# Kernel optimization log

Measured on AMD Instinct MI355X. Metric: run time of the kernel, lower is better.

## Reference

```python
import jax, jax.numpy as jnp
import numpy as np

B, S, D = 8, 2048, 1024
N = 256          # state_dim
H = 512          # selector_hidden
E = 8            # num_experts


def murmurhash3_finalizer(token_ids):
    # Torch code works in int64 but masks to 32 bits after each multiply and
    # values stay non-negative, so it is exactly uint32 wrapping arithmetic.
    x = token_ids.astype(jnp.uint32)
    x = x ^ (x >> 16)
    x = x * jnp.uint32(2246822507)
    x = x ^ (x >> 13)
    x = x * jnp.uint32(3266489909)
    x = x ^ (x >> 16)
    return x


def setup_inputs() -> dict:
    key = jax.random.key(0)
    ks = jax.random.split(key, 7)
    scale = 0.02
    return {
        "x": jax.random.normal(ks[0], (B, S, D), dtype=jnp.float32),
        "token_ids": jax.random.randint(ks[1], (B, S), 0, 50257, dtype=jnp.int32),
        "Win": jax.random.normal(ks[2], (E, N, D), dtype=jnp.float32) * scale,      # in_proj.weight per expert
        "Wsin": jax.random.normal(ks[3], (E, H, D), dtype=jnp.float32) * scale,     # selector_in.weight
        "Wsout": jax.random.normal(ks[4], (E, 4 * N, H), dtype=jnp.float32) * scale,  # selector_out.weight
        "Wout": jax.random.normal(ks[5], (E, D, N), dtype=jnp.float32) * scale,     # out_proj.weight
        "dparam": jnp.ones((E, N), dtype=jnp.float32),                              # per-expert d
    }


def _forward(x, Win, Wsin, Wsout, Wout, dparam, token_ids):
    b, s, d = x.shape
    e_num, n, _ = Win.shape
    routes = (murmurhash3_finalizer(token_ids) % jnp.uint32(e_num)).astype(jnp.int32)  # (B,S)

    # Per-token expert projections, selected by hash route (masked accumulation
    # over the small fixed expert count; honors per-token routing).
    u = jnp.zeros((b, s, n), x.dtype)
    a = jnp.zeros((b, s, n), x.dtype)
    bg = jnp.zeros((b, s, n), x.dtype)
    c = jnp.zeros((b, s, n), x.dtype)
    dg = jnp.zeros((b, s, n), x.dtype)
    for e in range(e_num):
        m = (routes == e)[..., None]
        u = jnp.where(m, jnp.einsum('bsd,nd->bsn', x, Win[e]), u)
        sh = jax.nn.silu(jnp.einsum('bsd,hd->bsh', x, Wsin[e]))
        sel = jnp.einsum('bsh,oh->bso', sh, Wsout[e])       # (B,S,4N)
        ar, br, cr, dr = jnp.split(sel, 4, axis=-1)
        a = jnp.where(m, jax.nn.sigmoid(ar), a)
        bg = jnp.where(m, jnp.tanh(br), bg)
        c = jnp.where(m, jnp.tanh(cr), c)
        dg = jnp.where(m, jax.nn.sigmoid(dr), dg)

    dvec = dparam[routes]              # (B,S,N) expert d param per token
    skip = dvec * dg * u               # residual term, state-independent

    bidx = jnp.arange(b)

    def step(states, inp):
        # states: (B,E,N) per-expert hidden state per batch row
        route_t, u_t, a_t, b_t, c_t, skip_t = inp
        h_prev = states[bidx, route_t]                 # (B,N)
        h = a_t * h_prev + b_t * u_t
        states = states.at[bidx, route_t].set(h)       # only routed expert updates
        y = c_t * h + skip_t
        return states, y

    xs = (routes.swapaxes(0, 1), u.swapaxes(0, 1), a.swapaxes(0, 1),
          bg.swapaxes(0, 1), c.swapaxes(0, 1), skip.swapaxes(0, 1))
    states0 = jnp.zeros((b, e_num, n), x.dtype)
    _, ys = jax.lax.scan(step, states0, xs)            # ys: (S,B,N)
    y = ys.swapaxes(0, 1)                              # (B,S,N)

    out = jnp.zeros((b, s, d), x.dtype)
    for e in range(e_num):
        m = (routes == e)[..., None]
        out = jnp.where(m, jnp.einsum('bsn,dn->bsd', y, Wout[e]), out)
    return out


def reference(x, token_ids, Win, Wsin, Wsout, Wout, dparam):
    return _forward(x, Win, Wsin, Wsout, Wout, dparam, token_ids)
```

## Files before the change

### kernel.cpp

```cpp
#include <hip/hip_runtime.h>


#define TOKS 16384
#define RPAD 16512
#define DD   1024
#define NN   256
#define HH   512
#define MAXTILES  136
#define MAXCHUNKS 1088
#define CHUNK 16

typedef short short8 __attribute__((ext_vector_type(8)));
typedef float floatx4 __attribute__((ext_vector_type(4)));
typedef _Float16 half_t;

#define AS_GLOBAL __attribute__((address_space(1)))
#define AS_LDS    __attribute__((address_space(3)))

__device__ __forceinline__ void gl_lds16(const void* g, void* l) {
    __builtin_amdgcn_global_load_lds((const AS_GLOBAL void*)g, (AS_LDS void*)l, 16, 0, 0);
}

__device__ __forceinline__ unsigned short f2bf(float f) {
    union { float f; unsigned u; } c; c.f = f;
    unsigned r = c.u + 0x7FFF + ((c.u >> 16) & 1);
    return (unsigned short)(r >> 16);
}
__device__ __forceinline__ int route_of(int token) {
    unsigned x = (unsigned)token;
    x ^= x >> 16; x *= 2246822507u; x ^= x >> 13; x *= 3266489909u; x ^= x >> 16;
    return (int)(x & 7u);
}
__device__ __forceinline__ float sigm(float v) { return 1.0f / (1.0f + __expf(-v)); }
__device__ __forceinline__ float ftanh(float v) {
    float e = __expf(2.0f * v);
    return 1.0f - 2.0f / (e + 1.0f);
}

__global__ void k_route(const int* __restrict__ tok, int* __restrict__ cnt) {
    int b = blockIdx.x, tid = threadIdx.x;
    __shared__ int lc[256 * 8];
    #pragma unroll
    for (int e = 0; e < 8; e++) lc[tid * 8 + e] = 0;
    #pragma unroll
    for (int i = 0; i < 8; i++) {
        int e = route_of(tok[b * 2048 + tid * 8 + i]);
        lc[tid * 8 + e]++;
    }
    __syncthreads();
    if (tid < 8) {
        int s = 0;
        for (int t = 0; t < 256; t++) s += lc[t * 8 + tid];
        cnt[b * 8 + tid] = s;
    }
}

__global__ void k_offsets(const int* __restrict__ cnt, int* __restrict__ grpoff,
                          int* __restrict__ tileE, int* __restrict__ tileS,
                          int* __restrict__ tileR,
                          int* __restrict__ cGrp, int* __restrict__ cStart,
                          int* __restrict__ cLen, int* __restrict__ gBase,
                          int* __restrict__ meta) {
    __shared__ int sc[64], ce[8], eoff[9], etile[9], gb[65], go[64];
    int tid = threadIdx.x;
    if (tid < 64) sc[tid] = cnt[tid];
    __syncthreads();
    if (tid < 8) { int s = 0; for (int b = 0; b < 8; b++) s += sc[b * 8 + tid]; ce[tid] = s; }
    __syncthreads();
    if (tid == 0) {
        eoff[0] = 0; etile[0] = 0;
        for (int e = 0; e < 8; e++) {
            eoff[e + 1] = eoff[e] + ce[e];
            etile[e + 1] = etile[e] + (ce[e] + 127) / 128;
        }
        meta[0] = etile[8];
        gb[0] = 0;
        for (int g = 0; g < 64; g++) gb[g + 1] = gb[g] + (sc[g] + CHUNK - 1) / CHUNK;
        meta[1] = gb[64];
    }
    __syncthreads();
    if (tid < 64) {
        int b = tid >> 3, e = tid & 7;
        int run = eoff[e];
        for (int b2 = 0; b2 < b; b2++) run += sc[b2 * 8 + e];
        go[tid] = run;
        grpoff[tid] = run;
    }
    __syncthreads();
    if (tid < 8) {
        int e = tid, st = eoff[e], c = ce[e], t0 = etile[e];
        for (int i = 0, k = 0; i < c; i += 128, k++) {
            tileE[t0 + k] = e; tileS[t0 + k] = st + i;
            tileR[t0 + k] = (c - i < 128) ? (c - i) : 128;
        }
    }
    if (tid < 64) {
        int g = tid, n = sc[g], base = gb[g], s0 = go[g];
        gBase[g] = base;
        for (int i = 0, c = 0; i < n; i += CHUNK, c++) {
            cGrp[base + c] = g;
            cStart[base + c] = s0 + i;
            cLen[base + c] = (n - i < CHUNK) ? (n - i) : CHUNK;
        }
    }
}

__global__ void k_scatter(const int* __restrict__ tok, const int* __restrict__ grpoff,
                          int* __restrict__ perm) {
    int b = blockIdx.x, tid = threadIdx.x;
    __shared__ int lh[8 * 256];
    int r[8];
    int myc[8] = {0,0,0,0,0,0,0,0};
    #pragma unroll
    for (int i = 0; i < 8; i++) {
        int e = route_of(tok[b * 2048 + tid * 8 + i]);
        r[i] = e; myc[e]++;
    }
    #pragma unroll
    for (int e = 0; e < 8; e++) lh[e * 256 + tid] = myc[e];
    __syncthreads();
    for (int e = 0; e < 8; e++) {
        for (int off = 1; off < 256; off <<= 1) {
            int add = (tid >= off) ? lh[e * 256 + tid - off] : 0;
            __syncthreads();
            lh[e * 256 + tid] += add;
            __syncthreads();
        }
    }
    int basep[8];
    #pragma unroll
    for (int e = 0; e < 8; e++) basep[e] = grpoff[b * 8 + e] + lh[e * 256 + tid] - myc[e];
    #pragma unroll
    for (int i = 0; i < 8; i++) {
        int e = r[i];
        perm[basep[e]++] = b * 2048 + tid * 8 + i;
    }
}

__global__ void k_cvtw(const float* __restrict__ Win, const float* __restrict__ Wsin,
                       const float* __restrict__ Wsout, const float* __restrict__ Wout,
                       unsigned short* __restrict__ W12, unsigned short* __restrict__ Wso,
                       unsigned short* __restrict__ Wo) {
    const int C12 = 8 * 768 * 1024 / 4, CSO = 8 * 1024 * 512 / 4, CWO = 8 * 1024 * 256 / 4;
    int c = blockIdx.x * 256 + threadIdx.x;
    float4 v; unsigned short* dst;
    if (c < C12) {
        int d = c * 4;
        int e = d / (768 * 1024);
        int rem = d - e * (768 * 1024);
        int r = rem >> 10, k = rem & 1023;
        const float* src = (r < 256) ? (Win + (((size_t)e * 256 + r) << 10) + k)
                                     : (Wsin + (((size_t)e * 512 + (r - 256)) << 10) + k);
        v = *(const float4*)src;
        dst = W12 + d;
    } else if (c < C12 + CSO) {
        int d = (c - C12) * 4;
        v = *(const float4*)(Wsout + d);
        dst = Wso + d;
    } else if (c < C12 + CSO + CWO) {
        int d = (c - C12 - CSO) * 4;
        v = *(const float4*)(Wout + d);
        dst = Wo + d;
    } else return;
    ushort4 o;
    o.x = f2bf(v.x); o.y = f2bf(v.y); o.z = f2bf(v.z); o.w = f2bf(v.w);
    *(ushort4*)dst = o;
}

__global__ void k_gather(const float* __restrict__ x, const int* __restrict__ perm,
                         unsigned short* __restrict__ Xs, unsigned short* __restrict__ SHb,
                         unsigned short* __restrict__ Yb) {
    int r = blockIdx.x, t = threadIdx.x;
    if (r < TOKS) {
        int tok = perm[r];
        float4 v = *(const float4*)(x + (size_t)tok * 1024 + t * 4);
        ushort4 o;
        o.x = f2bf(v.x); o.y = f2bf(v.y); o.z = f2bf(v.z); o.w = f2bf(v.w);
        *(ushort4*)(Xs + (size_t)r * 1024 + t * 4) = o;
    } else {
        ushort4 z = {0, 0, 0, 0};
        *(ushort4*)(Xs + (size_t)r * 1024 + t * 4) = z;
        if (t < 128) *(ushort4*)(SHb + (size_t)r * 512 + t * 4) = z;
        if (t < 64)  *(ushort4*)(Yb + (size_t)r * 256 + t * 4) = z;
    }
}

template<int MODE, int KD>
__global__ __launch_bounds__(256, 5)
void k_mfma(const unsigned short* __restrict__ A, const unsigned short* __restrict__ Bw,
            const int* __restrict__ perm, const float* __restrict__ dparam,
            half_t* __restrict__ Ub, unsigned short* __restrict__ SHb,
            half_t* __restrict__ Aa, half_t* __restrict__ Wg,
            half_t* __restrict__ Cc, half_t* __restrict__ Sk,
            float* __restrict__ out,
            const int* __restrict__ tileE, const int* __restrict__ tileS,
            const int* __restrict__ tileR, const int* __restrict__ meta) {
    const int mt = blockIdx.y;
    if (mt >= meta[0]) return;
    const int e = tileE[mt], pos0 = tileS[mt], rows = tileR[mt];
    const int col0 = blockIdx.x * 128;
    const int tid = threadIdx.x;
    const int w = tid >> 6, lane = tid & 63, quad = lane >> 4, l15 = lane & 15;
    const int wm = w & 1, wn = w >> 1;
    constexpr int NOUT = (MODE == 0) ? 768 : 1024;
    constexpr int NK = KD / 32;

    __shared__ unsigned short As[2][128 * 32];
    __shared__ unsigned short Bs[2][128 * 32];

    const int r0 = tid >> 2;
    const int c8s = ((tid & 3) ^ ((tid >> 3) & 3)) * 8;
    const unsigned short* ga = A + (size_t)(pos0 + r0) * KD + c8s;
    const unsigned short* gb = Bw + ((size_t)e * NOUT + col0 + r0) * KD + c8s;

    floatx4 acc[4][4] = {};

    const int sq = (quad ^ ((l15 >> 1) & 3)) * 8;
    int aoff[4], boff[4];
    #pragma unroll
    for (int i = 0; i < 4; i++) aoff[i] = (wm * 64 + i * 16 + l15) * 32 + sq;
    #pragma unroll
    for (int j = 0; j < 4; j++) boff[j] = (wn * 64 + j * 16 + l15) * 32 + sq;

    #define STAGE(buf, k0) do { \
        gl_lds16(ga + (k0),                    As[buf] + w * 512); \
        gl_lds16(ga + (size_t)64 * KD + (k0),  As[buf] + 2048 + w * 512); \
        gl_lds16(gb + (k0),                    Bs[buf] + w * 512); \
        gl_lds16(gb + (size_t)64 * KD + (k0),  Bs[buf] + 2048 + w * 512); \
    } while (0)

    STAGE(0, 0);
    for (int kt = 0; kt < NK; kt++) {
        const int cur = kt & 1;
        if (kt + 1 < NK) {
            STAGE(cur ^ 1, (kt + 1) * 32);
            asm volatile("s_waitcnt vmcnt(4)" ::: "memory");
        } else {
            asm volatile("s_waitcnt vmcnt(0)" ::: "memory");
        }
        __builtin_amdgcn_s_barrier();
        asm volatile("" ::: "memory");
        short8 af[4], bf[4];
        #pragma unroll
        for (int i = 0; i < 4; i++) af[i] = *(const short8*)(As[cur] + aoff[i]);
        #pragma unroll
        for (int j = 0; j < 4; j++) bf[j] = *(const short8*)(Bs[cur] + boff[j]);
        #pragma unroll
        for (int i = 0; i < 4; i++)
            #pragma unroll
            for (int j = 0; j < 4; j++)
                acc[i][j] = __builtin_amdgcn_mfma_f32_16x16x32_bf16(af[i], bf[j], acc[i][j], 0, 0, 0);
        if (kt + 1 < NK) {
            asm volatile("s_waitcnt lgkmcnt(0)" ::: "memory");
            __builtin_amdgcn_s_barrier();
        }
    }
    #undef STAGE
    asm volatile("" ::: "memory");

    #pragma unroll
    for (int i = 0; i < 4; i++) {
        #pragma unroll
        for (int r = 0; r < 4; r++) {
            int m = wm * 64 + i * 16 + quad * 4 + r;
            if (m >= rows) continue;
            size_t row = (size_t)(pos0 + m);
            if (MODE == 0) {
                if (col0 < 256) {
                    #pragma unroll
                    for (int j = 0; j < 4; j++) {
                        int n = col0 + wn * 64 + j * 16 + l15;
                        Ub[row * 256 + n] = (half_t)acc[i][j][r];
                    }
                } else {
                    #pragma unroll
                    for (int j = 0; j < 4; j++) {
                        int n = col0 - 256 + wn * 64 + j * 16 + l15;
                        float v = acc[i][j][r];
                        SHb[row * 512 + n] = f2bf(v * sigm(v));
                    }
                }
            } else if (MODE == 1) {
                int region = col0 >> 8;
                #pragma unroll
                for (int j = 0; j < 4; j++) {
                    int n0 = (col0 & 255) + wn * 64 + j * 16 + l15;
                    size_t idx = row * 256 + (size_t)n0;
                    float v = acc[i][j][r];
                    if (region == 0) {
                        Aa[idx] = (half_t)sigm(v);
                    } else if (region == 1) {
                        Wg[idx] = (half_t)(ftanh(v) * (float)Ub[idx]);
                    } else if (region == 2) {
                        Cc[idx] = (half_t)ftanh(v);
                    } else {
                        Sk[idx] = (half_t)(dparam[e * 256 + n0] * sigm(v) * (float)Ub[idx]);
                    }
                }
            } else {
                int tok = perm[row];
                #pragma unroll
                for (int j = 0; j < 4; j++) {
                    int n = col0 + wn * 64 + j * 16 + l15;
                    out[(size_t)tok * 1024 + n] = acc[i][j][r];
                }
            }
        }
    }
}

__global__ void k_scanA(const half_t* __restrict__ Aa, const half_t* __restrict__ Wg,
                        const int* __restrict__ cStart, const int* __restrict__ cLen,
                        const int* __restrict__ meta,
                        float* __restrict__ SA, float* __restrict__ SQ) {
    int id = blockIdx.x;
    if (id >= meta[1]) return;
    int t = threadIdx.x;
    int s0 = cStart[id], L = cLen[id];
    size_t idx = (size_t)s0 * 256 + t;
    float p = 1.0f, q = 0.0f;
    for (int i = 0; i < L; i++) {
        float a = (float)Aa[idx], ww = (float)Wg[idx];
        q = a * q + ww;
        p *= a;
        idx += 256;
    }
    SA[(size_t)id * 256 + t] = p;
    SQ[(size_t)id * 256 + t] = q;
}

__global__ void k_scanB(const float* __restrict__ SA, const float* __restrict__ SQ,
                        const int* __restrict__ gBase, const int* __restrict__ cnt,
                        float* __restrict__ Hin) {
    int g = blockIdx.x, t = threadIdx.x;
    int base = gBase[g], nch = (cnt[g] + CHUNK - 1) / CHUNK;
    float h = 0.0f;
    for (int c = 0; c < nch; c++) {
        size_t k = (size_t)(base + c) * 256 + t;
        Hin[k] = h;
        h = SA[k] * h + SQ[k];
    }
}

__global__ void k_scanC(const half_t* __restrict__ Aa, const half_t* __restrict__ Wg,
                        const half_t* __restrict__ Cc, const half_t* __restrict__ Sk,
                        const int* __restrict__ cStart, const int* __restrict__ cLen,
                        const int* __restrict__ meta, const float* __restrict__ Hin,
                        unsigned short* __restrict__ Yb) {
    int id = blockIdx.x;
    if (id >= meta[1]) return;
    int t = threadIdx.x;
    int s0 = cStart[id], L = cLen[id];
    float h = Hin[(size_t)id * 256 + t];
    size_t idx = (size_t)s0 * 256 + t;
    for (int i = 0; i < L; i++) {
        float a = (float)Aa[idx], ww = (float)Wg[idx];
        float c = (float)Cc[idx], sk = (float)Sk[idx];
        h = a * h + ww;
        Yb[idx] = f2bf(c * h + sk);
        idx += 256;
    }
}

extern "C" void kernel_launch(void* const* d_in, const int* in_sizes, int n_in,
                              void* d_out, int out_size, void* d_ws, size_t ws_size,
                              hipStream_t stream) {
    const float* xin   = (const float*)d_in[0];
    const int*   tok   = (const int*)d_in[1];
    const float* Win   = (const float*)d_in[2];
    const float* Wsin  = (const float*)d_in[3];
    const float* Wsout = (const float*)d_in[4];
    const float* Wout  = (const float*)d_in[5];
    const float* dpar  = (const float*)d_in[6];
    float* out = (float*)d_out;

    size_t off = 0;
    char* base = (char*)d_ws;
    auto alloc = [&](size_t bytes) -> void* {
        void* p = base + off;
        off += (bytes + 255) & ~(size_t)255;
        return p;
    };
    half_t*         Ub  = (half_t*)alloc((size_t)RPAD * NN * 2);
    unsigned short* SHb = (unsigned short*)alloc((size_t)RPAD * HH * 2);
    unsigned short* Xs  = (unsigned short*)alloc((size_t)RPAD * DD * 2);
    unsigned short* Yb  = (unsigned short*)alloc((size_t)RPAD * NN * 2);
    half_t* Aa = (half_t*)alloc((size_t)TOKS * NN * 2);
    half_t* Wg = (half_t*)alloc((size_t)TOKS * NN * 2);
    half_t* Cc = (half_t*)alloc((size_t)TOKS * NN * 2);
    half_t* Sk = (half_t*)alloc((size_t)TOKS * NN * 2);
    unsigned short* W12 = (unsigned short*)alloc((size_t)8 * 768 * 1024 * 2);
    unsigned short* Wso = (unsigned short*)alloc((size_t)8 * 1024 * 512 * 2);
    unsigned short* Wo  = (unsigned short*)alloc((size_t)8 * 1024 * 256 * 2);
    float* SA  = (float*)alloc((size_t)MAXCHUNKS * 256 * 4);
    float* SQ  = (float*)alloc((size_t)MAXCHUNKS * 256 * 4);
    float* Hin = (float*)alloc((size_t)MAXCHUNKS * 256 * 4);
    int* perm   = (int*)alloc(TOKS * 4);
    int* cnt    = (int*)alloc(64 * 4);
    int* grpoff = (int*)alloc(64 * 4);
    int* tileE  = (int*)alloc(MAXTILES * 4);
    int* tileS  = (int*)alloc(MAXTILES * 4);
    int* tileR  = (int*)alloc(MAXTILES * 4);
    int* cGrp   = (int*)alloc(MAXCHUNKS * 4);
    int* cStart = (int*)alloc(MAXCHUNKS * 4);
    int* cLen   = (int*)alloc(MAXCHUNKS * 4);
    int* gBase  = (int*)alloc(64 * 4);
    int* meta   = (int*)alloc(16 * 4);

    k_route<<<8, 256, 0, stream>>>(tok, cnt);
    k_offsets<<<1, 256, 0, stream>>>(cnt, grpoff, tileE, tileS, tileR,
                                     cGrp, cStart, cLen, gBase, meta);
    k_scatter<<<8, 256, 0, stream>>>(tok, grpoff, perm);
    k_cvtw<<<12288, 256, 0, stream>>>(Win, Wsin, Wsout, Wout, W12, Wso, Wo);
    k_gather<<<RPAD, 256, 0, stream>>>(xin, perm, Xs, SHb, Yb);

    k_mfma<0, 1024><<<dim3(6, MAXTILES), 256, 0, stream>>>(Xs, W12, perm, dpar,
        Ub, SHb, Aa, Wg, Cc, Sk, out, tileE, tileS, tileR, meta);
    k_mfma<1, 512><<<dim3(8, MAXTILES), 256, 0, stream>>>(SHb, Wso, perm, dpar,
        Ub, SHb, Aa, Wg, Cc, Sk, out, tileE, tileS, tileR, meta);

    k_scanA<<<MAXCHUNKS, 256, 0, stream>>>(Aa, Wg, cStart, cLen, meta, SA, SQ);
    k_scanB<<<64, 256, 0, stream>>>(SA, SQ, gBase, cnt, Hin);
    k_scanC<<<MAXCHUNKS, 256, 0, stream>>>(Aa, Wg, Cc, Sk, cStart, cLen, meta, Hin, Yb);

    k_mfma<2, 256><<<dim3(8, MAXTILES), 256, 0, stream>>>(Yb, Wo, perm, dpar,
        Ub, SHb, Aa, Wg, Cc, Sk, out, tileE, tileS, tileR, meta);
}
```

Baseline: 366.1 us.

## Keep A tile resident in LDS and stream weight column blocks per workgroup

The grouped MFMA GEMM now loads the whole K-extent of the activation tile into LDS once. Each workgroup then loops over several 128-column weight blocks through a triple-buffered B pipeline, instead of reloading A for every column block. The first GEMM switches to 64-row tiles, one workgroup per tile covering all 768 outputs. The other two use 512-thread workgroups covering 4 column blocks each. This cuts redundant activation traffic and launch width, at the cost of large LDS footprints, lower occupancy, and fewer workgroups, which may leave CUs underused.

```diff
diff --git a/kernel.cpp b/kernel.cpp
--- a/kernel.cpp
+++ b/kernel.cpp
@@ -7,6 +7,7 @@
 #define NN   256
 #define HH   512
 #define MAXTILES  136
+#define MAXT64    272
 #define MAXCHUNKS 1088
 #define CHUNK 16
 
@@ -58,22 +59,26 @@
 __global__ void k_offsets(const int* __restrict__ cnt, int* __restrict__ grpoff,
                           int* __restrict__ tileE, int* __restrict__ tileS,
                           int* __restrict__ tileR,
+                          int* __restrict__ tE64, int* __restrict__ tS64,
+                          int* __restrict__ tR64,
                           int* __restrict__ cGrp, int* __restrict__ cStart,
                           int* __restrict__ cLen, int* __restrict__ gBase,
                           int* __restrict__ meta) {
-    __shared__ int sc[64], ce[8], eoff[9], etile[9], gb[65], go[64];
+    __shared__ int sc[64], ce[8], eoff[9], etile[9], et64[9], gb[65], go[64];
     int tid = threadIdx.x;
     if (tid < 64) sc[tid] = cnt[tid];
     __syncthreads();
     if (tid < 8) { int s = 0; for (int b = 0; b < 8; b++) s += sc[b * 8 + tid]; ce[tid] = s; }
     __syncthreads();
     if (tid == 0) {
-        eoff[0] = 0; etile[0] = 0;
+        eoff[0] = 0; etile[0] = 0; et64[0] = 0;
         for (int e = 0; e < 8; e++) {
             eoff[e + 1] = eoff[e] + ce[e];
             etile[e + 1] = etile[e] + (ce[e] + 127) / 128;
+            et64[e + 1] = et64[e] + (ce[e] + 63) / 64;
         }
         meta[0] = etile[8];
+        meta[2] = et64[8];
         gb[0] = 0;
         for (int g = 0; g < 64; g++) gb[g + 1] = gb[g] + (sc[g] + CHUNK - 1) / CHUNK;
         meta[1] = gb[64];
@@ -92,6 +97,13 @@
         for (int i = 0, k = 0; i < c; i += 128, k++) {
             tileE[t0 + k] = e; tileS[t0 + k] = st + i;
             tileR[t0 + k] = (c - i < 128) ? (c - i) : 128;
+        }
+    }
+    if (tid >= 8 && tid < 16) {
+        int e = tid - 8, st = eoff[e], c = ce[e], t0 = et64[e];
+        for (int i = 0, k = 0; i < c; i += 64, k++) {
+            tE64[t0 + k] = e; tS64[t0 + k] = st + i;
+            tR64[t0 + k] = (c - i < 64) ? (c - i) : 64;
         }
     }
     if (tid < 64) {
@@ -185,128 +197,153 @@
     }
 }
 
-template<int MODE, int KD>
-__global__ __launch_bounds__(256, 5)
+template<int MODE, int KD, int BM, int THR, int COLS_PB, int MIDX, int MINW>
+__global__ __launch_bounds__(THR, MINW)
 void k_mfma(const unsigned short* __restrict__ A, const unsigned short* __restrict__ Bw,
             const int* __restrict__ perm, const float* __restrict__ dparam,
             half_t* __restrict__ Ub, unsigned short* __restrict__ SHb,
             half_t* __restrict__ Aa, half_t* __restrict__ Wg,
             half_t* __restrict__ Cc, half_t* __restrict__ Sk,
             float* __restrict__ out,
-            const int* __restrict__ tileE, const int* __restrict__ tileS,
-            const int* __restrict__ tileR, const int* __restrict__ meta) {
-    const int mt = blockIdx.y;
-    if (mt >= meta[0]) return;
-    const int e = tileE[mt], pos0 = tileS[mt], rows = tileR[mt];
-    const int col0 = blockIdx.x * 128;
+            const int* __restrict__ tE, const int* __restrict__ tS,
+            const int* __restrict__ tR, const int* __restrict__ meta) {
+    constexpr int NKS  = KD / 32;
+    constexpr int LOGK = (NKS == 32) ? 5 : (NKS == 16) ? 4 : 3;
+    constexpr int ASTR = BM * 32;
+    constexpr int NOUT = (MODE == 0) ? 768 : 1024;
+    constexpr int WM   = BM / 64;
+    constexpr int TOT  = COLS_PB * NKS;
+    constexpr int BL   = 8192 / (THR * 16);
+
+    const int mt = (MODE == 0) ? blockIdx.x : blockIdx.y;
+    if (mt >= meta[MIDX]) return;
+    const int e = tE[mt], pos0 = tS[mt], rows = tR[mt];
+    const int colbase = (MODE == 0) ? 0 : blockIdx.x * (COLS_PB * 128);
     const int tid = threadIdx.x;
     const int w = tid >> 6, lane = tid & 63, quad = lane >> 4, l15 = lane & 15;
-    const int wm = w & 1, wn = w >> 1;
-    constexpr int NOUT = (MODE == 0) ? 768 : 1024;
-    constexpr int NK = KD / 32;
-
-    __shared__ unsigned short As[2][128 * 32];
-    __shared__ unsigned short Bs[2][128 * 32];
+    const int wm = (WM == 2) ? (w & 1) : 0;
+    const int wn = (WM == 2) ? (w >> 1) : w;
+
+    __shared__ unsigned short Ares[NKS * ASTR];
+    __shared__ unsigned short Bs[3][128 * 32];
 
     const int r0 = tid >> 2;
     const int c8s = ((tid & 3) ^ ((tid >> 3) & 3)) * 8;
-    const unsigned short* ga = A + (size_t)(pos0 + r0) * KD + c8s;
-    const unsigned short* gb = Bw + ((size_t)e * NOUT + col0 + r0) * KD + c8s;
-
-    floatx4 acc[4][4] = {};
+    const unsigned short* ga  = A + (size_t)(pos0 + r0) * KD + c8s;
+    const unsigned short* gbb = Bw + ((size_t)e * NOUT + colbase + r0) * KD + c8s;
 
     const int sq = (quad ^ ((l15 >> 1) & 3)) * 8;
-    int aoff[4], boff[4];
+    int aoff[4], boff[2];
     #pragma unroll
     for (int i = 0; i < 4; i++) aoff[i] = (wm * 64 + i * 16 + l15) * 32 + sq;
     #pragma unroll
-    for (int j = 0; j < 4; j++) boff[j] = (wn * 64 + j * 16 + l15) * 32 + sq;
-
-    #define STAGE(buf, k0) do { \
-        gl_lds16(ga + (k0),                    As[buf] + w * 512); \
-        gl_lds16(ga + (size_t)64 * KD + (k0),  As[buf] + 2048 + w * 512); \
-        gl_lds16(gb + (k0),                    Bs[buf] + w * 512); \
-        gl_lds16(gb + (size_t)64 * KD + (k0),  Bs[buf] + 2048 + w * 512); \
+    for (int j = 0; j < 2; j++) boff[j] = (wn * 32 + j * 16 + l15) * 32 + sq;
+
+    #define STAGE_B(buf, s) do { \
+        int cc_ = (s) >> LOGK, ks_ = (s) & (NKS - 1); \
+        const unsigned short* p_ = gbb + (size_t)cc_ * (128 * KD) + ks_ * 32; \
+        gl_lds16(p_, Bs[buf] + w * 512); \
+        if (BL == 2) gl_lds16(p_ + (size_t)64 * KD, Bs[buf] + 2048 + w * 512); \
     } while (0)
 
-    STAGE(0, 0);
-    for (int kt = 0; kt < NK; kt++) {
-        const int cur = kt & 1;
-        if (kt + 1 < NK) {
-            STAGE(cur ^ 1, (kt + 1) * 32);
-            asm volatile("s_waitcnt vmcnt(4)" ::: "memory");
-        } else {
-            asm volatile("s_waitcnt vmcnt(0)" ::: "memory");
+    #pragma unroll
+    for (int s = 0; s < NKS; s++)
+        gl_lds16(ga + s * 32, Ares + s * ASTR + w * 512);
+    STAGE_B(0, 0);
+    STAGE_B(1, 1);
+    asm volatile("s_waitcnt vmcnt(0)" ::: "memory");
+    __builtin_amdgcn_s_barrier();
+
+    floatx4 acc[4][2] = {};
+
+    #pragma unroll 1
+    for (int s = 0; s < TOT; s++) {
+        const int ks = s & (NKS - 1);
+        const int buf = s % 3;
+        if (s > 1) {
+            if (s < TOT - 1) {
+                if (BL == 2) asm volatile("s_waitcnt vmcnt(2)" ::: "memory");
+                else         asm volatile("s_waitcnt vmcnt(1)" ::: "memory");
+            } else {
+                asm volatile("s_waitcnt vmcnt(0)" ::: "memory");
+            }
         }
         __builtin_amdgcn_s_barrier();
         asm volatile("" ::: "memory");
-        short8 af[4], bf[4];
+        if (s + 2 < TOT) STAGE_B((s + 2) % 3, s + 2);
+        short8 af[4], bf[2];
         #pragma unroll
-        for (int i = 0; i < 4; i++) af[i] = *(const short8*)(As[cur] + aoff[i]);
+        for (int i = 0; i < 4; i++) af[i] = *(const short8*)(Ares + ks * ASTR + aoff[i]);
         #pragma unroll
-        for (int j = 0; j < 4; j++) bf[j] = *(const short8*)(Bs[cur] + boff[j]);
+        for (int j = 0; j < 2; j++) bf[j] = *(const short8*)(Bs[buf] + boff[j]);
         #pragma unroll
         for (int i = 0; i < 4; i++)
             #pragma unroll
-            for (int j = 0; j < 4; j++)
+            for (int j = 0; j < 2; j++)
                 acc[i][j] = __builtin_amdgcn_mfma_f32_16x16x32_bf16(af[i], bf[j], acc[i][j], 0, 0, 0);
-        if (kt + 1 < NK) {
-            asm volatile("s_waitcnt lgkmcnt(0)" ::: "memory");
-            __builtin_amdgcn_s_barrier();
-        }
-    }
-    #undef STAGE
-    asm volatile("" ::: "memory");
-
-    #pragma unroll
-    for (int i = 0; i < 4; i++) {
-        #pragma unroll
-        for (int r = 0; r < 4; r++) {
-            int m = wm * 64 + i * 16 + quad * 4 + r;
-            if (m >= rows) continue;
-            size_t row = (size_t)(pos0 + m);
-            if (MODE == 0) {
-                if (col0 < 256) {
-                    #pragma unroll
-                    for (int j = 0; j < 4; j++) {
-                        int n = col0 + wn * 64 + j * 16 + l15;
-                        Ub[row * 256 + n] = (half_t)acc[i][j][r];
-                    }
-                } else {
-                    #pragma unroll
-                    for (int j = 0; j < 4; j++) {
-                        int n = col0 - 256 + wn * 64 + j * 16 + l15;
-                        float v = acc[i][j][r];
-                        SHb[row * 512 + n] = f2bf(v * sigm(v));
+        asm volatile("s_waitcnt lgkmcnt(0)" ::: "memory");
+        __builtin_amdgcn_sched_barrier(0);
+
+        if (ks == NKS - 1) {
+            const int cc = s >> LOGK;
+            const int col0 = colbase + cc * 128;
+            #pragma unroll
+            for (int i = 0; i < 4; i++) {
+                #pragma unroll
+                for (int r = 0; r < 4; r++) {
+                    int m = wm * 64 + i * 16 + quad * 4 + r;
+                    if (m >= rows) continue;
+                    size_t row = (size_t)(pos0 + m);
+                    if (MODE == 0) {
+                        if (col0 < 256) {
+                            #pragma unroll
+                            for (int j = 0; j < 2; j++) {
+                                int n = col0 + wn * 32 + j * 16 + l15;
+                                Ub[row * 256 + n] = (half_t)acc[i][j][r];
+                            }
+                        } else {
+                            #pragma unroll
+                            for (int j = 0; j < 2; j++) {
+                                int n = col0 - 256 + wn * 32 + j * 16 + l15;
+                                float v = acc[i][j][r];
+                                SHb[row * 512 + n] = f2bf(v * sigm(v));
+                            }
+                        }
+                    } else if (MODE == 1) {
+                        int region = col0 >> 8;
+                        #pragma unroll
+                        for (int j = 0; j < 2; j++) {
+                            int n0 = (col0 & 255) + wn * 32 + j * 16 + l15;
+                            size_t idx = row * 256 + (size_t)n0;
+                            float v = acc[i][j][r];
+                            if (region == 0) {
+                                Aa[idx] = (half_t)sigm(v);
+                            } else if (region == 1) {
+                                Wg[idx] = (half_t)(ftanh(v) * (float)Ub[idx]);
+                            } else if (region == 2) {
+                                Cc[idx] = (half_t)ftanh(v);
+                            } else {
+                                Sk[idx] = (half_t)(dparam[e * 256 + n0] * sigm(v) * (float)Ub[idx]);
+                            }
+                        }
+                    } else {
+                        int tok = perm[row];
+                        #pragma unroll
+                        for (int j = 0; j < 2; j++) {
+                            int n = col0 + wn * 32 + j * 16 + l15;
+                            out[(size_t)tok * 1024 + n] = acc[i][j][r];
+                        }
                     }
                 }
-            } else if (MODE == 1) {
-                int region = col0 >> 8;
+            }
+            #pragma unroll
+            for (int i = 0; i < 4; i++)
                 #pragma unroll
-                for (int j = 0; j < 4; j++) {
-                    int n0 = (col0 & 255) + wn * 64 + j * 16 + l15;
-                    size_t idx = row * 256 + (size_t)n0;
-                    float v = acc[i][j][r];
-                    if (region == 0) {
-                        Aa[idx] = (half_t)sigm(v);
-                    } else if (region == 1) {
-                        Wg[idx] = (half_t)(ftanh(v) * (float)Ub[idx]);
-                    } else if (region == 2) {
-                        Cc[idx] = (half_t)ftanh(v);
-                    } else {
-                        Sk[idx] = (half_t)(dparam[e * 256 + n0] * sigm(v) * (float)Ub[idx]);
-                    }
-                }
-            } else {
-                int tok = perm[row];
-                #pragma unroll
-                for (int j = 0; j < 4; j++) {
-                    int n = col0 + wn * 64 + j * 16 + l15;
-                    out[(size_t)tok * 1024 + n] = acc[i][j][r];
-                }
-            }
-        }
-    }
+                for (int j = 0; j < 2; j++)
+                    acc[i][j] = (floatx4){0.0f, 0.0f, 0.0f, 0.0f};
+        }
+    }
+    #undef STAGE_B
 }
 
 __global__ void k_scanA(const half_t* __restrict__ Aa, const half_t* __restrict__ Wg,
@@ -401,6 +438,9 @@
     int* tileE  = (int*)alloc(MAXTILES * 4);
     int* tileS  = (int*)alloc(MAXTILES * 4);
     int* tileR  = (int*)alloc(MAXTILES * 4);
+    int* tE64   = (int*)alloc(MAXT64 * 4);
+    int* tS64   = (int*)alloc(MAXT64 * 4);
+    int* tR64   = (int*)alloc(MAXT64 * 4);
     int* cGrp   = (int*)alloc(MAXCHUNKS * 4);
     int* cStart = (int*)alloc(MAXCHUNKS * 4);
     int* cLen   = (int*)alloc(MAXCHUNKS * 4);
@@ -409,20 +449,21 @@
 
     k_route<<<8, 256, 0, stream>>>(tok, cnt);
     k_offsets<<<1, 256, 0, stream>>>(cnt, grpoff, tileE, tileS, tileR,
+                                     tE64, tS64, tR64,
                                      cGrp, cStart, cLen, gBase, meta);
     k_scatter<<<8, 256, 0, stream>>>(tok, grpoff, perm);
     k_cvtw<<<12288, 256, 0, stream>>>(Win, Wsin, Wsout, Wout, W12, Wso, Wo);
     k_gather<<<RPAD, 256, 0, stream>>>(xin, perm, Xs, SHb, Yb);
 
-    k_mfma<0, 1024><<<dim3(6, MAXTILES), 256, 0, stream>>>(Xs, W12, perm, dpar,
-        Ub, SHb, Aa, Wg, Cc, Sk, out, tileE, tileS, tileR, meta);
-    k_mfma<1, 512><<<dim3(8, MAXTILES), 256, 0, stream>>>(SHb, Wso, perm, dpar,
-        Ub, SHb, Aa, Wg, Cc, Sk, out, tileE, tileS, tileR, meta);
+    k_mfma<0, 1024, 64, 256, 6, 2, 1><<<MAXT64, 256, 0, stream>>>(
+        Xs, W12, perm, dpar, Ub, SHb, Aa, Wg, Cc, Sk, out, tE64, tS64, tR64, meta);
+    k_mfma<1, 512, 128, 512, 4, 0, 2><<<dim3(2, MAXTILES), 512, 0, stream>>>(
+        SHb, Wso, perm, dpar, Ub, SHb, Aa, Wg, Cc, Sk, out, tileE, tileS, tileR, meta);
 
     k_scanA<<<MAXCHUNKS, 256, 0, stream>>>(Aa, Wg, cStart, cLen, meta, SA, SQ);
     k_scanB<<<64, 256, 0, stream>>>(SA, SQ, gBase, cnt, Hin);
     k_scanC<<<MAXCHUNKS, 256, 0, stream>>>(Aa, Wg, Cc, Sk, cStart, cLen, meta, Hin, Yb);
 
-    k_mfma<2, 256><<<dim3(8, MAXTILES), 256, 0, stream>>>(Yb, Wo, perm, dpar,
-        Ub, SHb, Aa, Wg, Cc, Sk, out, tileE, tileS, tileR, meta);
-}
+    k_mfma<2, 256, 128, 512, 4, 0, 2><<<dim3(2, MAXTILES), 512, 0, stream>>>(
+        Yb, Wo, perm, dpar, Ub, SHb, Aa, Wg, Cc, Sk, out, tileE, tileS, tileR, meta);
+}
```

Measured after the change: 619.6 us. 69.3% more time.
